# Optimization experiments

Measured on AMD Instinct MI355X. Metric: run time of the kernel, lower is better.

Reference implementation:

```python
import jax, jax.numpy as jnp
import numpy as np

H = 768
V = 21128
LN_EPS = 1e-12


def setup_inputs() -> dict:
    key = jax.random.key(0)
    ks = jax.random.split(key, 12)
    s = 0.02
    inp = {
        "cls_vec": jax.random.normal(ks[0], (8, H), dtype=jnp.float32),
        # LSTM (PyTorch layout: weight_ih (4H,H), weight_hh (4H,H), biases (4H,))
        "W_ih": s * jax.random.normal(ks[1], (4 * H, H), dtype=jnp.float32),
        "W_hh": s * jax.random.normal(ks[2], (4 * H, H), dtype=jnp.float32),
        "b_ih": s * jax.random.normal(ks[3], (4 * H,), dtype=jnp.float32),
        "b_hh": s * jax.random.normal(ks[4], (4 * H,), dtype=jnp.float32),
        # BertPredictionHeadTransform: dense(H,H) + gelu + LayerNorm
        "W_dense": s * jax.random.normal(ks[5], (H, H), dtype=jnp.float32),
        "b_dense": s * jax.random.normal(ks[6], (H,), dtype=jnp.float32),
        "ln_gamma": jnp.ones((H,), dtype=jnp.float32),
        "ln_beta": jnp.zeros((H,), dtype=jnp.float32),
        # decoder: Linear(H, V, bias=False) + separate bias param (tied)
        "W_voc": s * jax.random.normal(ks[7], (V, H), dtype=jnp.float32),
        "b_voc": jnp.zeros((V,), dtype=jnp.float32),
        "steps": 511,
    }
    return inp


def _lstm_cell(x, h, c, W_ih, W_hh, b_ih, b_hh):
    gates = x @ W_ih.T + b_ih + h @ W_hh.T + b_hh  # (B, 4H)
    i, f, g, o = jnp.split(gates, 4, axis=-1)
    i = jax.nn.sigmoid(i)
    f = jax.nn.sigmoid(f)
    g = jnp.tanh(g)
    o = jax.nn.sigmoid(o)
    c = f * c + i * g
    h = o * jnp.tanh(c)
    return h, c


def _head(x, W_dense, b_dense, ln_gamma, ln_beta, W_voc, b_voc):
    t = jax.nn.gelu(x @ W_dense.T + b_dense, approximate=False)
    mu = jnp.mean(t, axis=-1, keepdims=True)
    var = jnp.mean(jnp.square(t - mu), axis=-1, keepdims=True)
    t = (t - mu) * jax.lax.rsqrt(var + LN_EPS) * ln_gamma + ln_beta
    return t @ W_voc.T + b_voc  # (B, V)


def reference(cls_vec, W_ih, W_hh, b_ih, b_hh, W_dense, b_dense,
              ln_gamma, ln_beta, W_voc, b_voc, steps):
    B = cls_vec.shape[0]
    zeros = jnp.zeros((B, H), dtype=cls_vec.dtype)
    # decoder_out, (h_1, c_1) = self.decoder(cls_vec.unsqueeze(1))
    h, c = _lstm_cell(cls_vec, zeros, zeros, W_ih, W_hh, b_ih, b_hh)

    def step(carry, _):
        h, c = carry
        h, c = _lstm_cell(carry[0], h, c, W_ih, W_hh, b_ih, b_hh)
        logits = _head(h, W_dense, b_dense, ln_gamma, ln_beta, W_voc, b_voc)
        return (h, c), logits

    (h, c), logits = jax.lax.scan(step, (h, c), None, length=steps)
    return logits  # (steps, B, V)
```

## Files before the change

kernel.cpp:

```cpp
#include <hip/hip_runtime.h>
#include <hip/hip_bf16.h>
#include <cstdint>

#define HD 768
#define VOC 21128
#define VOCP 21248
#define NSTEPS 511
#define MROWS 4088
#define MPAD 4096
#define NBL 192

typedef float f32x4 __attribute__((ext_vector_type(4)));
typedef short short8 __attribute__((ext_vector_type(8)));

#define OFF_HW    768
#define OFF_HALLB 49920ULL
#define OFF_DT    6341376ULL
#define OFF_WDB   12632832ULL
#define OFF_WV    13812480ULL
#define PADH 772

__device__ __forceinline__ unsigned short f2bf(float x) {
  unsigned u = __float_as_uint(x);
  u += 0x7FFFu + ((u >> 16) & 1u);
  return (unsigned short)(u >> 16);
}
__device__ __forceinline__ float bf2f(unsigned short u) {
  return __uint_as_float(((unsigned)u) << 16);
}

__device__ __forceinline__ void gl_lds16(const void* g, void* l) {
  __builtin_amdgcn_global_load_lds(
      (const __attribute__((address_space(1))) void*)g,
      (__attribute__((address_space(3))) void*)l, 16, 0, 0);
}

__device__ __forceinline__ void st_u32(uint32_t* p, uint32_t v) {
  __hip_atomic_store(p, v, __ATOMIC_RELAXED, __HIP_MEMORY_SCOPE_AGENT);
}
__device__ __forceinline__ uint32_t ld_u32(const uint32_t* p) {
  return __hip_atomic_load(p, __ATOMIC_RELAXED, __HIP_MEMORY_SCOPE_AGENT);
}

__device__ __forceinline__ float swz8(float x) {
  return __int_as_float(__builtin_amdgcn_ds_swizzle(__float_as_int(x), 0x201F));
}
__device__ __forceinline__ float swz16(float x) {
  return __int_as_float(__builtin_amdgcn_ds_swizzle(__float_as_int(x), 0x401F));
}

__device__ __forceinline__ float sigf(float x) {
  return __builtin_amdgcn_rcpf(1.f + __expf(-x));
}
__device__ __forceinline__ float tanhf_fast(float x) {
  float ax = fabsf(x);
  float e = __expf(-2.f * ax);
  float t = (1.f - e) * __builtin_amdgcn_rcpf(1.f + e);
  return copysignf(t, x);
}

__global__ __launch_bounds__(256) void prep_kernel(
    const float* __restrict__ Wd, unsigned short* __restrict__ WdB,
    const float* __restrict__ Wv, unsigned short* __restrict__ WvB,
    uint32_t* __restrict__ hw) {
  unsigned idx = blockIdx.x * 256 + threadIdx.x;
  unsigned stride = gridDim.x * 256;
  for (unsigned i = idx; i < 12288; i += stride) hw[i] = 0;
  for (unsigned i = idx; i < HD * HD; i += stride) WdB[i] = f2bf(Wd[i]);
  const unsigned NV = (unsigned)VOCP * HD, NVr = (unsigned)VOC * HD;
  for (unsigned i = idx; i < NV; i += stride)
    WvB[i] = f2bf(i < NVr ? Wv[i] : 0.f);
}

__global__ __launch_bounds__(256) void lstm_kernel(
    const float* __restrict__ cls, const float* __restrict__ Wih,
    const float* __restrict__ Whh, const float* __restrict__ bih,
    const float* __restrict__ bhh, uint32_t* __restrict__ hw,
    unsigned short* __restrict__ HallB) {
  __shared__ float h_lds[8 * PADH];
  __shared__ float red[4][2][16][8];
  __shared__ float sbias[16];
  const int t = threadIdx.x;
  const int blk = blockIdx.x;
  const int p_ = t & 7;
  const int s_ = t >> 3;
  const int ks = s_ * 24;
  const int r0 = 2 * p_, r1 = r0 + 1;
  const int grow0 = (r0 >> 2) * HD + blk * 4 + (r0 & 3);
  const int grow1 = (r1 >> 2) * HD + blk * 4 + (r1 & 3);
  float w0[24], w1[24];
#pragma unroll
  for (int j = 0; j < 24; ++j) {
    w0[j] = Wih[(size_t)grow0 * HD + ks + j];
    w1[j] = Wih[(size_t)grow1 * HD + ks + j];
  }
  if (t < 16) {
    int gr = (t >> 2) * HD + blk * 4 + (t & 3);
    sbias[t] = bih[gr] + bhh[gr];
  }
  float cstate = 0.f;
  const int lane = t & 63, wv = t >> 6, hf = (lane >> 5);

  auto do_step = [&](uint32_t* __restrict__ hw_out, int tag,
                     unsigned short* __restrict__ hall_row) {
    float acc0[8], acc1[8];
#pragma unroll
    for (int b = 0; b < 8; ++b) { acc0[b] = 0.f; acc1[b] = 0.f; }
#pragma unroll
    for (int b = 0; b < 8; ++b) {
      const float* hb = &h_lds[b * PADH + ks];
#pragma unroll
      for (int j4 = 0; j4 < 6; ++j4) {
        f32x4 hv = *reinterpret_cast<const f32x4*>(hb + j4 * 4);
#pragma unroll
        for (int e = 0; e < 4; ++e) {
          acc0[b] = fmaf(w0[j4 * 4 + e], hv[e], acc0[b]);
          acc1[b] = fmaf(w1[j4 * 4 + e], hv[e], acc1[b]);
        }
      }
    }
#pragma unroll
    for (int b = 0; b < 8; ++b) {
      acc0[b] += swz8(acc0[b]);  acc0[b] += swz16(acc0[b]);
      acc1[b] += swz8(acc1[b]);  acc1[b] += swz16(acc1[b]);
    }
    if ((lane & 31) < 8) {
#pragma unroll
      for (int b = 0; b < 8; ++b) {
        red[wv][hf][r0][b] = acc0[b];
        red[wv][hf][r1][b] = acc1[b];
      }
    }
    __syncthreads();
    if (t < 32) {
      int ul = t >> 3, b = t & 7;
      float gs[4];
#pragma unroll
      for (int g = 0; g < 4; ++g) {
        int r = g * 4 + ul;
        float s = sbias[r];
#pragma unroll
        for (int w2 = 0; w2 < 4; ++w2) s += red[w2][0][r][b] + red[w2][1][r][b];
        gs[g] = s;
      }
      float iv = sigf(gs[0]);
      float fv = sigf(gs[1]);
      float gv = tanhf_fast(gs[2]);
      float ov = sigf(gs[3]);
      cstate = fv * cstate + iv * gv;
      float hn = ov * tanhf_fast(cstate);
      union { _Float16 f; unsigned short u; } cv;
      cv.f = (_Float16)hn;
      st_u32(&hw_out[(blk * 4 + ul) * 8 + b],
             ((uint32_t)tag << 16) | (uint32_t)cv.u);
      if (hall_row) hall_row[(size_t)b * HD + blk * 4 + ul] = f2bf(hn);
    }
  };

  for (int i = t; i < 1536; i += 256) {
    int b = i / 192, c4 = i - b * 192;
    *reinterpret_cast<f32x4*>(&h_lds[b * PADH + c4 * 4]) =
        reinterpret_cast<const f32x4*>(cls)[i];
  }
  __syncthreads();
  do_step(hw + 6144, 1, nullptr);
#pragma unroll
  for (int j = 0; j < 24; ++j) {
    w0[j] += Whh[(size_t)grow0 * HD + ks + j];
    w1[j] += Whh[(size_t)grow1 * HD + ks + j];
  }
  for (int s = 1; s <= NSTEPS; ++s) {
    const uint32_t* src = hw + (s & 1) * 6144;
    uint32_t w[24];
    bool ok;
    do {
      ok = true;
#pragma unroll
      for (int k = 0; k < 24; ++k) {
        w[k] = ld_u32(&src[t + k * 256]);
        if ((w[k] >> 16) != (uint32_t)s) ok = false;
      }
    } while (!ok);
#pragma unroll
    for (int k = 0; k < 24; ++k) {
      int f = t + k * 256;
      union { unsigned short u; _Float16 f16; } cv;
      cv.u = (unsigned short)(w[k] & 0xFFFFu);
      h_lds[(f & 7) * PADH + (f >> 3)] = (float)cv.f16;
    }
    __syncthreads();
    do_step(hw + ((s + 1) & 1) * 6144, s + 1,
            HallB + (size_t)(s - 1) * (8 * HD));
  }
}

__global__ __launch_bounds__(256) void head_mm_kernel(
    const unsigned short* __restrict__ Ha, const unsigned short* __restrict__ Wb,
    const float* __restrict__ bd, unsigned short* __restrict__ DT) {
  __shared__ unsigned short As[128 * 64];
  __shared__ unsigned short Bs[128 * 64];
  const int t = threadIdx.x;
  const int lane = t & 63, wid = t >> 6;
  const int wm = wid >> 1, wn = wid & 1;
  const int m0 = blockIdx.y * 128, n0 = blockIdx.x * 128;
  const int lrow = lane & 15, lgrp = lane >> 4;
  f32x4 acc[4][4] = {};
  for (int kt = 0; kt < HD; kt += 64) {
#pragma unroll
    for (int it = 0; it < 4; ++it) {
      int slot = it * 256 + t;
      int row = slot >> 3, g = slot & 7;
      int sg = g ^ (row & 7);
      const unsigned short* sa = Ha + (size_t)(m0 + row) * HD + kt + sg * 8;
      const unsigned short* sb = Wb + (size_t)(n0 + row) * HD + kt + sg * 8;
      unsigned short* da = &As[(it * 256 + wid * 64) * 8];
      unsigned short* db = &Bs[(it * 256 + wid * 64) * 8];
      gl_lds16(sa, da);
      gl_lds16(sb, db);
    }
    __syncthreads();
#pragma unroll
    for (int kk = 0; kk < 2; ++kk) {
      short8 af[4], bfr[4];
#pragma unroll
      for (int i = 0; i < 4; ++i) {
        int row = wm * 64 + i * 16 + lrow;
        int gg = (kk * 4 + lgrp) ^ (row & 7);
        af[i] = *reinterpret_cast<const short8*>(&As[row * 64 + gg * 8]);
      }
#pragma unroll
      for (int j = 0; j < 4; ++j) {
        int row = wn * 64 + j * 16 + lrow;
        int gg = (kk * 4 + lgrp) ^ (row & 7);
        bfr[j] = *reinterpret_cast<const short8*>(&Bs[row * 64 + gg * 8]);
      }
#pragma unroll
      for (int i = 0; i < 4; ++i)
#pragma unroll
        for (int j = 0; j < 4; ++j)
          acc[i][j] = __builtin_amdgcn_mfma_f32_16x16x32_bf16(af[i], bfr[j], acc[i][j], 0, 0, 0);
    }
    __syncthreads();
  }
#pragma unroll
  for (int j = 0; j < 4; ++j) {
    int col = n0 + wn * 64 + j * 16 + lrow;
    float bv = bd[col];
#pragma unroll
    for (int i = 0; i < 4; ++i) {
      int rbase = m0 + wm * 64 + i * 16 + lgrp * 4;
#pragma unroll
      for (int e = 0; e < 4; ++e) {
        int row = rbase + e;
        if (row < MROWS) {
          float x = acc[i][j][e] + bv;
          float g = 0.5f * x * (1.f + erff(x * 0.7071067811865476f));
          DT[(size_t)row * HD + col] = f2bf(g);
        }
      }
    }
  }
}

__global__ __launch_bounds__(256) void ln_kernel(
    unsigned short* __restrict__ DT, const float* __restrict__ gamma,
    const float* __restrict__ beta) {
  __shared__ float rbuf[4][16];
  __shared__ float mu_s[16], rs_s[16];
  const int t = threadIdx.x;
  const int r0 = blockIdx.x * 16;
  float a0[16], a1[16], a2[16];
#pragma unroll
  for (int r = 0; r < 16; ++r) {
    size_t ro = (size_t)(r0 + r) * HD;
    a0[r] = bf2f(DT[ro + t]);
    a1[r] = bf2f(DT[ro + t + 256]);
    a2[r] = bf2f(DT[ro + t + 512]);
  }
  float g0 = gamma[t], g1 = gamma[t + 256], g2 = gamma[t + 512];
  float be0 = beta[t], be1 = beta[t + 256], be2 = beta[t + 512];
  float ps[16];
  const int lane = t & 63, wv = t >> 6;
#pragma unroll
  for (int r = 0; r < 16; ++r) ps[r] = a0[r] + a1[r] + a2[r];
#pragma unroll
  for (int r = 0; r < 16; ++r)
#pragma unroll
    for (int m = 1; m < 64; m <<= 1) ps[r] += __shfl_xor(ps[r], m);
  if (lane == 0) {
#pragma unroll
    for (int r = 0; r < 16; ++r) rbuf[wv][r] = ps[r];
  }
  __syncthreads();
  if (t < 16) mu_s[t] = (rbuf[0][t] + rbuf[1][t] + rbuf[2][t] + rbuf[3][t]) * (1.f / HD);
  __syncthreads();
#pragma unroll
  for (int r = 0; r < 16; ++r) {
    float mu = mu_s[r];
    float d0 = a0[r] - mu, d1 = a1[r] - mu, d2 = a2[r] - mu;
    ps[r] = d0 * d0 + d1 * d1 + d2 * d2;
  }
#pragma unroll
  for (int r = 0; r < 16; ++r)
#pragma unroll
    for (int m = 1; m < 64; m <<= 1) ps[r] += __shfl_xor(ps[r], m);
  if (lane == 0) {
#pragma unroll
    for (int r = 0; r < 16; ++r) rbuf[wv][r] = ps[r];
  }
  __syncthreads();
  if (t < 16)
    rs_s[t] = 1.f / sqrtf((rbuf[0][t] + rbuf[1][t] + rbuf[2][t] + rbuf[3][t]) * (1.f / HD) + 1e-12f);
  __syncthreads();
#pragma unroll
  for (int r = 0; r < 16; ++r) {
    float mu = mu_s[r], rs = rs_s[r];
    size_t ro = (size_t)(r0 + r) * HD;
    DT[ro + t]       = f2bf((a0[r] - mu) * rs * g0 + be0);
    DT[ro + t + 256] = f2bf((a1[r] - mu) * rs * g1 + be1);
    DT[ro + t + 512] = f2bf((a2[r] - mu) * rs * g2 + be2);
  }
}

__global__ __launch_bounds__(256) void gemm_kernel(
    const unsigned short* __restrict__ Tm, const unsigned short* __restrict__ Wv,
    const float* __restrict__ bvoc, float* __restrict__ out) {
  __shared__ unsigned short As[128 * 64];
  __shared__ unsigned short Bs[128 * 64];
  const int t = threadIdx.x;
  const int lane = t & 63, wid = t >> 6;
  const int wm = wid >> 1, wn = wid & 1;
  const int nbx = VOCP / 128;
  int lid = blockIdx.y * nbx + blockIdx.x;
  int swz = (lid & 7) * ((nbx * (MPAD / 128)) >> 3) + (lid >> 3);
  const int m0 = (swz / nbx) * 128, n0 = (swz % nbx) * 128;
  const int lrow = lane & 15, lgrp = lane >> 4;
  f32x4 acc[4][4] = {};
  for (int kt = 0; kt < HD; kt += 64) {
#pragma unroll
    for (int it = 0; it < 4; ++it) {
      int slot = it * 256 + t;
      int row = slot >> 3, g = slot & 7;
      int sg = g ^ (row & 7);
      const unsigned short* sa = Tm + (size_t)(m0 + row) * HD + kt + sg * 8;
      const unsigned short* sb = Wv + (size_t)(n0 + row) * HD + kt + sg * 8;
      unsigned short* da = &As[(it * 256 + wid * 64) * 8];
      unsigned short* db = &Bs[(it * 256 + wid * 64) * 8];
      gl_lds16(sa, da);
      gl_lds16(sb, db);
    }
    __syncthreads();
#pragma unroll
    for (int kk = 0; kk < 2; ++kk) {
      short8 af[4], bfr[4];
#pragma unroll
      for (int i = 0; i < 4; ++i) {
        int row = wm * 64 + i * 16 + lrow;
        int gg = (kk * 4 + lgrp) ^ (row & 7);
        af[i] = *reinterpret_cast<const short8*>(&As[row * 64 + gg * 8]);
      }
#pragma unroll
      for (int j = 0; j < 4; ++j) {
        int row = wn * 64 + j * 16 + lrow;
        int gg = (kk * 4 + lgrp) ^ (row & 7);
        bfr[j] = *reinterpret_cast<const short8*>(&Bs[row * 64 + gg * 8]);
      }
#pragma unroll
      for (int i = 0; i < 4; ++i)
#pragma unroll
        for (int j = 0; j < 4; ++j)
          acc[i][j] = __builtin_amdgcn_mfma_f32_16x16x32_bf16(af[i], bfr[j], acc[i][j], 0, 0, 0);
    }
    __syncthreads();
  }
#pragma unroll
  for (int j = 0; j < 4; ++j) {
    int col = n0 + wn * 64 + j * 16 + lrow;
    bool cok = col < VOC;
    float bv = cok ? bvoc[col] : 0.f;
#pragma unroll
    for (int i = 0; i < 4; ++i) {
      int rbase = m0 + wm * 64 + i * 16 + lgrp * 4;
#pragma unroll
      for (int e = 0; e < 4; ++e) {
        int row = rbase + e;
        if (cok && row < MROWS) out[(size_t)row * VOC + col] = acc[i][j][e] + bv;
      }
    }
  }
}

extern "C" void kernel_launch(void* const* d_in, const int* in_sizes, int n_in,
                              void* d_out, int out_size, void* d_ws, size_t ws_size,
                              hipStream_t stream) {
  (void)in_sizes; (void)n_in; (void)out_size; (void)ws_size;
  const float* cls  = (const float*)d_in[0];
  const float* Wih  = (const float*)d_in[1];
  const float* Whh  = (const float*)d_in[2];
  const float* bih  = (const float*)d_in[3];
  const float* bhh  = (const float*)d_in[4];
  const float* Wd   = (const float*)d_in[5];
  const float* bd   = (const float*)d_in[6];
  const float* gmm  = (const float*)d_in[7];
  const float* bet  = (const float*)d_in[8];
  const float* Wv   = (const float*)d_in[9];
  const float* bvoc = (const float*)d_in[10];
  char* ws = (char*)d_ws;
  uint32_t* hw = (uint32_t*)(ws + OFF_HW);
  unsigned short* HallB = (unsigned short*)(ws + OFF_HALLB);
  unsigned short* DT    = (unsigned short*)(ws + OFF_DT);
  unsigned short* WdB   = (unsigned short*)(ws + OFF_WDB);
  unsigned short* WvB   = (unsigned short*)(ws + OFF_WV);
  float* out = (float*)d_out;

  hipLaunchKernelGGL(prep_kernel, dim3(4096), dim3(256), 0, stream, Wd, WdB, Wv, WvB, hw);
  hipLaunchKernelGGL(lstm_kernel, dim3(NBL), dim3(256), 0, stream,
                     cls, Wih, Whh, bih, bhh, hw, HallB);
  hipLaunchKernelGGL(head_mm_kernel, dim3(HD / 128, MPAD / 128), dim3(256), 0, stream,
                     HallB, WdB, bd, DT);
  hipLaunchKernelGGL(ln_kernel, dim3(MPAD / 16), dim3(256), 0, stream,
                     DT, gmm, bet);
  hipLaunchKernelGGL(gemm_kernel, dim3(VOCP / 128, MPAD / 128), dim3(256), 0, stream,
                     DT, WvB, bvoc, out);
}
```

Baseline: 2.068 ms.

## Overlap weight bf16 conversion with LSTM and double-buffer 256x256 vocab GEMM

The weight-to-bf16 conversion moves into 64 extra blocks of the LSTM kernel, so it runs alongside the latency-bound serial recurrence instead of as a separate launch before it. The vocab GEMM switches to 256x256 tiles with 512 threads and double-buffered LDS, prefetching the next K slice with explicit vmcnt waits and raw barriers. This aims to hide global-load latency and raise reuse per tile. It costs more LDS (128KB) and accumulator registers, which lowers occupancy, and the extra blocks may contend with the LSTM's grid-wide synchronisation.

```diff
diff --git a/kernel.cpp b/kernel.cpp
--- a/kernel.cpp
+++ b/kernel.cpp
@@ -59,28 +59,30 @@
   return copysignf(t, x);
 }
 
-__global__ __launch_bounds__(256) void prep_kernel(
-    const float* __restrict__ Wd, unsigned short* __restrict__ WdB,
-    const float* __restrict__ Wv, unsigned short* __restrict__ WvB,
-    uint32_t* __restrict__ hw) {
-  unsigned idx = blockIdx.x * 256 + threadIdx.x;
-  unsigned stride = gridDim.x * 256;
-  for (unsigned i = idx; i < 12288; i += stride) hw[i] = 0;
-  for (unsigned i = idx; i < HD * HD; i += stride) WdB[i] = f2bf(Wd[i]);
-  const unsigned NV = (unsigned)VOCP * HD, NVr = (unsigned)VOC * HD;
-  for (unsigned i = idx; i < NV; i += stride)
-    WvB[i] = f2bf(i < NVr ? Wv[i] : 0.f);
+__global__ __launch_bounds__(256) void zero_hw_kernel(uint32_t* __restrict__ hw) {
+  hw[blockIdx.x * 256 + threadIdx.x] = 0;
 }
 
 __global__ __launch_bounds__(256) void lstm_kernel(
     const float* __restrict__ cls, const float* __restrict__ Wih,
     const float* __restrict__ Whh, const float* __restrict__ bih,
     const float* __restrict__ bhh, uint32_t* __restrict__ hw,
-    unsigned short* __restrict__ HallB) {
+    unsigned short* __restrict__ HallB,
+    const float* __restrict__ Wd, unsigned short* __restrict__ WdB,
+    const float* __restrict__ Wv, unsigned short* __restrict__ WvB) {
+  const int t = threadIdx.x;
+  if (blockIdx.x >= NBL) {
+    unsigned idx = (blockIdx.x - NBL) * 256 + t;
+    const unsigned stride = 64 * 256;
+    for (unsigned i = idx; i < HD * HD; i += stride) WdB[i] = f2bf(Wd[i]);
+    const unsigned NV = (unsigned)VOCP * HD, NVr = (unsigned)VOC * HD;
+    for (unsigned i = idx; i < NV; i += stride)
+      WvB[i] = f2bf(i < NVr ? Wv[i] : 0.f);
+    return;
+  }
   __shared__ float h_lds[8 * PADH];
   __shared__ float red[4][2][16][8];
   __shared__ float sbias[16];
-  const int t = threadIdx.x;
   const int blk = blockIdx.x;
   const int p_ = t & 7;
   const int s_ = t >> 3;
@@ -322,56 +324,65 @@
   }
 }
 
-__global__ __launch_bounds__(256) void gemm_kernel(
+__global__ __launch_bounds__(512) void gemm_kernel(
     const unsigned short* __restrict__ Tm, const unsigned short* __restrict__ Wv,
     const float* __restrict__ bvoc, float* __restrict__ out) {
-  __shared__ unsigned short As[128 * 64];
-  __shared__ unsigned short Bs[128 * 64];
+  __shared__ unsigned short As[2][256 * 64];
+  __shared__ unsigned short Bs[2][256 * 64];
   const int t = threadIdx.x;
   const int lane = t & 63, wid = t >> 6;
-  const int wm = wid >> 1, wn = wid & 1;
-  const int nbx = VOCP / 128;
+  const int wm = wid >> 2, wn = wid & 3;
+  const int nbx = VOCP / 256;
   int lid = blockIdx.y * nbx + blockIdx.x;
-  int swz = (lid & 7) * ((nbx * (MPAD / 128)) >> 3) + (lid >> 3);
-  const int m0 = (swz / nbx) * 128, n0 = (swz % nbx) * 128;
+  int swz = (lid & 7) * 166 + (lid >> 3);
+  const int m0 = (swz / nbx) * 256, n0 = (swz % nbx) * 256;
   const int lrow = lane & 15, lgrp = lane >> 4;
-  f32x4 acc[4][4] = {};
-  for (int kt = 0; kt < HD; kt += 64) {
-#pragma unroll
-    for (int it = 0; it < 4; ++it) {
-      int slot = it * 256 + t;
-      int row = slot >> 3, g = slot & 7;
+  f32x4 acc[8][4] = {};
+
+  auto stage = [&](int d, int kt) {
+#pragma unroll
+    for (int q = 0; q < 4; ++q) {
+      int s = q * 512 + wid * 64 + lane;
+      int row = s >> 3, g = s & 7;
       int sg = g ^ (row & 7);
-      const unsigned short* sa = Tm + (size_t)(m0 + row) * HD + kt + sg * 8;
-      const unsigned short* sb = Wv + (size_t)(n0 + row) * HD + kt + sg * 8;
-      unsigned short* da = &As[(it * 256 + wid * 64) * 8];
-      unsigned short* db = &Bs[(it * 256 + wid * 64) * 8];
-      gl_lds16(sa, da);
-      gl_lds16(sb, db);
-    }
-    __syncthreads();
+      unsigned short* da = &As[d][(q * 512 + wid * 64) * 8];
+      unsigned short* db = &Bs[d][(q * 512 + wid * 64) * 8];
+      gl_lds16(Tm + (size_t)(m0 + row) * HD + kt + sg * 8, da);
+      gl_lds16(Wv + (size_t)(n0 + row) * HD + kt + sg * 8, db);
+    }
+  };
+
+  stage(0, 0);
+  for (int it = 0; it < 12; ++it) {
+    int cur = it & 1;
+    if (it < 11) {
+      stage(cur ^ 1, (it + 1) * 64);
+      asm volatile("s_waitcnt vmcnt(8)" ::: "memory");
+    } else {
+      asm volatile("s_waitcnt vmcnt(0)" ::: "memory");
+    }
+    __builtin_amdgcn_s_barrier();
 #pragma unroll
     for (int kk = 0; kk < 2; ++kk) {
-      short8 af[4], bfr[4];
-#pragma unroll
-      for (int i = 0; i < 4; ++i) {
-        int row = wm * 64 + i * 16 + lrow;
-        int gg = (kk * 4 + lgrp) ^ (row & 7);
-        af[i] = *reinterpret_cast<const short8*>(&As[row * 64 + gg * 8]);
-      }
+      short8 bfr[4];
 #pragma unroll
       for (int j = 0; j < 4; ++j) {
         int row = wn * 64 + j * 16 + lrow;
         int gg = (kk * 4 + lgrp) ^ (row & 7);
-        bfr[j] = *reinterpret_cast<const short8*>(&Bs[row * 64 + gg * 8]);
-      }
-#pragma unroll
-      for (int i = 0; i < 4; ++i)
+        bfr[j] = *reinterpret_cast<const short8*>(&Bs[cur][row * 64 + gg * 8]);
+      }
+#pragma unroll
+      for (int i = 0; i < 8; ++i) {
+        int row = wm * 128 + i * 16 + lrow;
+        int gg = (kk * 4 + lgrp) ^ (row & 7);
+        short8 af = *reinterpret_cast<const short8*>(&As[cur][row * 64 + gg * 8]);
 #pragma unroll
         for (int j = 0; j < 4; ++j)
-          acc[i][j] = __builtin_amdgcn_mfma_f32_16x16x32_bf16(af[i], bfr[j], acc[i][j], 0, 0, 0);
-    }
-    __syncthreads();
+          acc[i][j] = __builtin_amdgcn_mfma_f32_16x16x32_bf16(af, bfr[j], acc[i][j], 0, 0, 0);
+      }
+    }
+    asm volatile("" ::: "memory");
+    __builtin_amdgcn_s_barrier();
   }
 #pragma unroll
   for (int j = 0; j < 4; ++j) {
@@ -379,8 +390,8 @@
     bool cok = col < VOC;
     float bv = cok ? bvoc[col] : 0.f;
 #pragma unroll
-    for (int i = 0; i < 4; ++i) {
-      int rbase = m0 + wm * 64 + i * 16 + lgrp * 4;
+    for (int i = 0; i < 8; ++i) {
+      int rbase = m0 + wm * 128 + i * 16 + lgrp * 4;
 #pragma unroll
       for (int e = 0; e < 4; ++e) {
         int row = rbase + e;
@@ -413,13 +424,13 @@
   unsigned short* WvB   = (unsigned short*)(ws + OFF_WV);
   float* out = (float*)d_out;
 
-  hipLaunchKernelGGL(prep_kernel, dim3(4096), dim3(256), 0, stream, Wd, WdB, Wv, WvB, hw);
-  hipLaunchKernelGGL(lstm_kernel, dim3(NBL), dim3(256), 0, stream,
-                     cls, Wih, Whh, bih, bhh, hw, HallB);
+  hipLaunchKernelGGL(zero_hw_kernel, dim3(48), dim3(256), 0, stream, hw);
+  hipLaunchKernelGGL(lstm_kernel, dim3(256), dim3(256), 0, stream,
+                     cls, Wih, Whh, bih, bhh, hw, HallB, Wd, WdB, Wv, WvB);
   hipLaunchKernelGGL(head_mm_kernel, dim3(HD / 128, MPAD / 128), dim3(256), 0, stream,
                      HallB, WdB, bd, DT);
   hipLaunchKernelGGL(ln_kernel, dim3(MPAD / 16), dim3(256), 0, stream,
                      DT, gmm, bet);
-  hipLaunchKernelGGL(gemm_kernel, dim3(VOCP / 128, MPAD / 128), dim3(256), 0, stream,
+  hipLaunchKernelGGL(gemm_kernel, dim3(VOCP / 256, MPAD / 256), dim3(512), 0, stream,
                      DT, WvB, bvoc, out);
 }
```

New measurement: 2.055 ms. No clear change (-0.7%).
